# Performance work log

Measured on AMD Instinct MI355X. Metric: run time of the kernel, lower is better.

The kernel has to match this reference:

```python
import jax, jax.numpy as jnp
import numpy as np

L, H, P = 131072, 128, 128
STEP_RESCALE = 1.0
CONJ_SYM = True


def setup_inputs() -> dict:
    key = jax.random.key(0)
    ks = jax.random.split(key, 9)
    x = jax.random.normal(ks[0], (L, H), jnp.float32)
    # stable SSM: real parts of Lambda must be negative so |dA| < 1
    A_real_log = -(0.5 + jax.random.uniform(ks[1], (P,), jnp.float32))
    A_imag = 3.0 * jax.random.normal(ks[2], (P,), jnp.float32)
    B_re = jax.random.normal(ks[3], (P, H), jnp.float32) / np.sqrt(H)
    B_im = jax.random.normal(ks[4], (P, H), jnp.float32) / np.sqrt(H)
    C_re = jax.random.normal(ks[5], (H, P), jnp.float32) / np.sqrt(P)
    C_im = jax.random.normal(ks[6], (H, P), jnp.float32) / np.sqrt(P)
    D = jax.random.normal(ks[7], (H,), jnp.float32)
    # softplus(inv_dt) small -> small timestep dt
    inv_dt = jax.random.normal(ks[8], (P,), jnp.float32) - 4.0
    return {"x": x, "A_real_log": A_real_log, "A_imag": A_imag,
            "B_re": B_re, "B_im": B_im, "C_re": C_re, "C_im": C_im,
            "D": D, "inv_dt": inv_dt}


def reference(x, A_real_log, A_imag, B_re, B_im, C_re, C_im, D, inv_dt):
    # A = Lambda (diagonal complex state matrix), shape (P,)
    A = A_real_log + 1j * A_imag
    dt = STEP_RESCALE * jax.nn.softplus(inv_dt)            # (P,)
    # bilinear (Tustin) discretization
    BL = 1.0 / (1.0 - 0.5 * dt * A)                        # (P,)
    dA = BL * (1.0 + 0.5 * dt * A)                         # (P,)
    B = B_re + 1j * B_im                                   # (P,H)
    dB = (BL * dt)[:, None] * B                            # (P,H)
    # input projection into state space: (L,P) complex
    Bu = jnp.einsum('lh,ph->lp', x + 0j, dB)
    # linear recurrence h_k = dA * h_{k-1} + Bu_k via parallel associative scan
    A_elems = jnp.broadcast_to(dA[None, :], Bu.shape)
    def binop(q1, q2):
        a1, b1 = q1
        a2, b2 = q2
        return a1 * a2, a2 * b1 + b2
    _, hs = jax.lax.associative_scan(binop, (A_elems, Bu), axis=0)  # (L,P)
    C = C_re + 1j * C_im                                   # (H,P)
    y = jnp.einsum('lp,hp->lh', hs, C).real                # (L,H)
    if CONJ_SYM:
        y = 2.0 * y
    return y + x * D[None, :]
```

## Files before the change

kernel.cpp:

```cpp
#include <hip/hip_runtime.h>

#define L_LEN 131072
#define H_DIM 128
#define P_DIM 128
#define SEG 32
#define NSEG (L_LEN / SEG)
#define ROWS 64
#define NBLK (L_LEN / ROWS)

typedef unsigned int uint32;
typedef unsigned short u16;
typedef short bf16x8 __attribute__((ext_vector_type(8)));
typedef float f32x4 __attribute__((ext_vector_type(4)));

constexpr size_t OFF_DA  = 0;
constexpr size_t OFF_E   = OFF_DA + 256;
constexpr size_t OFF_HIN = OFF_E + (size_t)NSEG * 256;
constexpr size_t OFF_W1F = OFF_HIN + (size_t)NSEG * 256;
constexpr size_t OFF_W2F = OFF_W1F + 32768;

__device__ __forceinline__ u16 f2bf(float v) {
    uint32 u = __builtin_bit_cast(uint32, v);
    uint32 r = u + 0x7FFFu + ((u >> 16) & 1u);
    return (u16)(r >> 16);
}
__device__ __forceinline__ float bf2f(u16 h) {
    uint32 u = ((uint32)h) << 16;
    return __builtin_bit_cast(float, u);
}
__device__ __forceinline__ uint32 cvtpk(float lo, float hi) {
    uint32 r;
    asm("v_cvt_pk_bf16_f32 %0, %1, %2" : "=v"(r) : "v"(lo), "v"(hi));
    return r;
}
__device__ __forceinline__ float2 cfma(float2 a, float2 h, float2 c) {
    float2 r;
    r.x = fmaf(a.x, h.x, fmaf(-a.y, h.y, c.x));
    r.y = fmaf(a.x, h.y, fmaf(a.y, h.x, c.y));
    return r;
}
__device__ __forceinline__ float2 cmul(float2 a, float2 b) {
    return make_float2(fmaf(a.x, b.x, -a.y * b.y), fmaf(a.x, b.y, a.y * b.x));
}
__device__ __forceinline__ float2 unpk(uint32 w) {
    return make_float2(bf2f((u16)(w & 0xffffu)), bf2f((u16)(w >> 16)));
}

__global__ void k0(const float* __restrict__ Arl, const float* __restrict__ Ai,
                   const float* __restrict__ invdt,
                   const float* __restrict__ Bre, const float* __restrict__ Bim,
                   const float* __restrict__ Cre, const float* __restrict__ Cim,
                   float* __restrict__ dA,
                   u16* __restrict__ W1F, u16* __restrict__ W2F) {
    int tid = blockIdx.x * 256 + threadIdx.x;
    int lane = tid & 63;
    int fb = (tid >> 6) & 63;
    int ar = lane & 15, aq = lane >> 4;
    ushort4 hiA, hiB, loA, loB;
    u16* dst;
    if (tid < 4096) {
        int kt = fb >> 4, cf = fb & 15;
        int q = cf * 16 + ar;
        int p = q >> 1, c = q & 1;
        int h0 = kt * 32 + aq * 8;
        float idt = invdt[p];
        float dt = (idt > 20.f) ? idt : log1pf(expf(idt));
        float arl = Arl[p], aii = Ai[p];
        float zr = 0.5f * dt * arl, zi = 0.5f * dt * aii;
        float drr = 1.f - zr, dii = -zi;
        float inv = 1.f / (drr * drr + dii * dii);
        float blr = drr * inv, bli = -dii * inv;
        float2 s = make_float2(blr * dt, bli * dt);
        u16 hh[8], ll[8];
        #pragma unroll
        for (int j = 0; j < 8; ++j) {
            float br = Bre[p * H_DIM + h0 + j], bi = Bim[p * H_DIM + h0 + j];
            float re = fmaf(s.x, br, -s.y * bi);
            float im = fmaf(s.x, bi,  s.y * br);
            float v = c ? im : re;
            u16 h = f2bf(v); hh[j] = h; ll[j] = f2bf(v - bf2f(h));
        }
        hiA = make_ushort4(hh[0], hh[1], hh[2], hh[3]);
        hiB = make_ushort4(hh[4], hh[5], hh[6], hh[7]);
        loA = make_ushort4(ll[0], ll[1], ll[2], ll[3]);
        loB = make_ushort4(ll[4], ll[5], ll[6], ll[7]);
        dst = W1F + fb * 1024 + lane * 8;
    } else {
        int kk = fb >> 3, cf = fb & 7;
        int h = cf * 16 + ar;
        int q0 = kk * 32 + aq * 8;
        u16 hh[8], ll[8];
        #pragma unroll
        for (int j = 0; j < 8; ++j) {
            int q = q0 + j; int p = q >> 1;
            float v = (q & 1) ? (-2.f * Cim[h * P_DIM + p]) : (2.f * Cre[h * P_DIM + p]);
            u16 hv = f2bf(v); hh[j] = hv; ll[j] = f2bf(v - bf2f(hv));
        }
        hiA = make_ushort4(hh[0], hh[1], hh[2], hh[3]);
        hiB = make_ushort4(hh[4], hh[5], hh[6], hh[7]);
        loA = make_ushort4(ll[0], ll[1], ll[2], ll[3]);
        loB = make_ushort4(ll[4], ll[5], ll[6], ll[7]);
        dst = W2F + fb * 1024 + lane * 8;
    }
    *(ushort4*)(dst)       = hiA;
    *(ushort4*)(dst + 4)   = hiB;
    *(ushort4*)(dst + 512) = loA;
    *(ushort4*)(dst + 516) = loB;

    if (blockIdx.x == 0 && threadIdx.x < 128) {
        int p = threadIdx.x;
        float idt = invdt[p];
        float dt = (idt > 20.f) ? idt : log1pf(expf(idt));
        float arl = Arl[p], aii = Ai[p];
        float zr = 0.5f * dt * arl, zi = 0.5f * dt * aii;
        float drr = 1.f - zr, dii = -zi;
        float inv = 1.f / (drr * drr + dii * dii);
        float blr = drr * inv, bli = -dii * inv;
        float nr = 1.f + zr, ni = zi;
        dA[2 * p]     = fmaf(blr, nr, -bli * ni);
        dA[2 * p + 1] = fmaf(blr, ni,  bli * nr);
    }
}

__global__ __launch_bounds__(256) void k1(const float* __restrict__ x,
                                          const u16* __restrict__ W1F,
                                          const float* __restrict__ dA,
                                          float* __restrict__ E) {
    __shared__ __align__(16) char smem[32768];
    u16* As_hi = (u16*)smem;
    u16* SB    = (u16*)smem;
    int t = threadIdx.x, lane = t & 63, wid = t >> 6;
    size_t l0 = (size_t)blockIdx.x * ROWS;
    int ar = lane & 15, aq = lane >> 4, ak = aq * 8;

    bf16x8 bhp[4][4];
    #pragma unroll
    for (int kt = 0; kt < 4; ++kt)
        #pragma unroll
        for (int nf = 0; nf < 4; ++nf)
            bhp[kt][nf] = *(const bf16x8*)(W1F + (size_t)(kt * 16 + wid * 4 + nf) * 1024 + lane * 8);

    float4 xv[8];
    #pragma unroll
    for (int j = 0; j < 8; ++j) {
        int f = j * 256 + t; int row = f >> 5, c4 = f & 31;
        xv[j] = *(const float4*)(x + (l0 + row) * H_DIM + c4 * 4);
    }
    #pragma unroll
    for (int j = 0; j < 8; ++j) {
        int f = j * 256 + t; int row = f >> 5, c4 = f & 31;
        uint2 wv;
        wv.x = cvtpk(xv[j].x, xv[j].y);
        wv.y = cvtpk(xv[j].z, xv[j].w);
        *(uint2*)&As_hi[row * 136 + c4 * 4] = wv;
    }
    __syncthreads();

    f32x4 acc[4][4];
    #pragma unroll
    for (int a = 0; a < 4; ++a)
        #pragma unroll
        for (int b = 0; b < 4; ++b) acc[a][b] = (f32x4)0.f;
    #pragma unroll
    for (int kt = 0; kt < 4; ++kt) {
        bf16x8 ah[4];
        #pragma unroll
        for (int mf = 0; mf < 4; ++mf)
            ah[mf] = *(const bf16x8*)&As_hi[(mf * 16 + ar) * 136 + kt * 32 + ak];
        #pragma unroll
        for (int nf = 0; nf < 4; ++nf)
            #pragma unroll
            for (int mf = 0; mf < 4; ++mf)
                acc[mf][nf] = __builtin_amdgcn_mfma_f32_16x16x32_bf16(ah[mf], bhp[kt][nf], acc[mf][nf], 0, 0, 0);
    }
    __syncthreads();

    int sr = aq * 4;
    #pragma unroll
    for (int mf = 0; mf < 4; ++mf)
        #pragma unroll
        for (int nf = 0; nf < 4; ++nf) {
            int col = wid * 64 + nf * 16 + ar;
            uint32 w01 = cvtpk(acc[mf][nf][0], acc[mf][nf][1]);
            uint32 w23 = cvtpk(acc[mf][nf][2], acc[mf][nf][3]);
            int r0 = mf * 16 + sr;
            SB[(r0 + 0) * 256 + (((col >> 3) ^ ((r0 + 0) & 7)) << 3) + (col & 7)] = (u16)w01;
            SB[(r0 + 1) * 256 + (((col >> 3) ^ ((r0 + 1) & 7)) << 3) + (col & 7)] = (u16)(w01 >> 16);
            SB[(r0 + 2) * 256 + (((col >> 3) ^ ((r0 + 2) & 7)) << 3) + (col & 7)] = (u16)w23;
            SB[(r0 + 3) * 256 + (((col >> 3) ^ ((r0 + 3) & 7)) << 3) + (col & 7)] = (u16)(w23 >> 16);
        }
    __syncthreads();

    {
        int s = t >> 7, p = t & 127;
        float2 a = ((const float2*)dA)[p];
        uint32 buf[SEG];
        #pragma unroll
        for (int i = 0; i < SEG; ++i) {
            int row = s * 32 + i;
            buf[i] = *(const uint32*)&SB[row * 256 + (((p >> 2) ^ (row & 7)) << 3) + (p & 3) * 2];
        }
        float2 e = make_float2(0.f, 0.f);
        #pragma unroll
        for (int i = 0; i < SEG; ++i) e = cfma(a, e, unpk(buf[i]));
        ((float2*)E)[((size_t)blockIdx.x * 2 + s) * P_DIM + p] = e;
    }
}

__global__ __launch_bounds__(256) void k3(const float* __restrict__ E,
                                          const float* __restrict__ dA,
                                          float* __restrict__ Hin) {
    __shared__ float4 wagg[4];
    int m = blockIdx.x, t = threadIdx.x;
    int lane = t & 63, w = t >> 6;
    float2 aS = ((const float2*)dA)[m];
    #pragma unroll
    for (int i = 0; i < 5; ++i) aS = cmul(aS, aS);
    const float2* e = (const float2*)E;
    float2 ebuf[16];
    #pragma unroll
    for (int i = 0; i < 16; ++i) ebuf[i] = e[(size_t)(t * 16 + i) * P_DIM + m];
    float2 Bv = ebuf[0];
    #pragma unroll
    for (int i = 1; i < 16; ++i) Bv = cfma(aS, Bv, ebuf[i]);
    float2 Av = aS;
    #pragma unroll
    for (int i = 0; i < 4; ++i) Av = cmul(Av, Av);

    #pragma unroll
    for (int d = 1; d < 64; d <<= 1) {
        float uAx = __shfl_up(Av.x, (unsigned)d, 64);
        float uAy = __shfl_up(Av.y, (unsigned)d, 64);
        float uBx = __shfl_up(Bv.x, (unsigned)d, 64);
        float uBy = __shfl_up(Bv.y, (unsigned)d, 64);
        if (lane >= d) {
            float2 uA = make_float2(uAx, uAy), uB = make_float2(uBx, uBy);
            Bv = cfma(Av, uB, Bv);
            Av = cmul(uA, Av);
        }
    }
    if (lane == 63) wagg[w] = make_float4(Av.x, Av.y, Bv.x, Bv.y);
    __syncthreads();
    float2 Pb = make_float2(0.f, 0.f);
    for (int i = 0; i < w; ++i) {
        float4 u = wagg[i];
        float2 Wa = make_float2(u.x, u.y), Wb = make_float2(u.z, u.w);
        Pb = cfma(Wa, Pb, Wb);
    }
    float eAx = __shfl_up(Av.x, 1u, 64), eAy = __shfl_up(Av.y, 1u, 64);
    float eBx = __shfl_up(Bv.x, 1u, 64), eBy = __shfl_up(Bv.y, 1u, 64);
    float2 eA = make_float2(eAx, eAy), eB = make_float2(eBx, eBy);
    if (lane == 0) { eA = make_float2(1.f, 0.f); eB = make_float2(0.f, 0.f); }
    float2 pre = cfma(eA, Pb, eB);
    float2* hin = (float2*)Hin;
    #pragma unroll
    for (int i = 0; i < 16; ++i) {
        hin[(size_t)(t * 16 + i) * P_DIM + m] = pre;
        pre = cfma(aS, pre, ebuf[i]);
    }
}

__global__ __launch_bounds__(256) void k4(const float* __restrict__ x,
                                          const u16* __restrict__ W1F,
                                          const u16* __restrict__ W2F,
                                          const float* __restrict__ dA,
                                          const float* __restrict__ Hin,
                                          const float* __restrict__ Dv,
                                          float* __restrict__ y) {
    __shared__ __align__(16) char smem[33280];
    u16*   As_hi = (u16*)smem;
    u16*   SB    = (u16*)smem;
    float* SBF   = (float*)smem;
    int t = threadIdx.x, lane = t & 63, wid = t >> 6;
    size_t l0 = (size_t)blockIdx.x * ROWS;
    int ar = lane & 15, aq = lane >> 4, ak = aq * 8;

    bf16x8 bhp[4][4];
    #pragma unroll
    for (int kt = 0; kt < 4; ++kt)
        #pragma unroll
        for (int nf = 0; nf < 4; ++nf)
            bhp[kt][nf] = *(const bf16x8*)(W1F + (size_t)(kt * 16 + wid * 4 + nf) * 1024 + lane * 8);

    float4 xv[8];
    #pragma unroll
    for (int j = 0; j < 8; ++j) {
        int f = j * 256 + t; int row = f >> 5, c4 = f & 31;
        xv[j] = *(const float4*)(x + (l0 + row) * H_DIM + c4 * 4);
    }
    #pragma unroll
    for (int j = 0; j < 8; ++j) {
        int f = j * 256 + t; int row = f >> 5, c4 = f & 31;
        uint2 wv;
        wv.x = cvtpk(xv[j].x, xv[j].y);
        wv.y = cvtpk(xv[j].z, xv[j].w);
        *(uint2*)&As_hi[row * 136 + c4 * 4] = wv;
    }
    __syncthreads();

    {
        f32x4 acc[4][4];
        #pragma unroll
        for (int a = 0; a < 4; ++a)
            #pragma unroll
            for (int b = 0; b < 4; ++b) acc[a][b] = (f32x4)0.f;
        #pragma unroll
        for (int kt = 0; kt < 4; ++kt) {
            bf16x8 ah[4];
            #pragma unroll
            for (int mf = 0; mf < 4; ++mf)
                ah[mf] = *(const bf16x8*)&As_hi[(mf * 16 + ar) * 136 + kt * 32 + ak];
            #pragma unroll
            for (int nf = 0; nf < 4; ++nf)
                #pragma unroll
                for (int mf = 0; mf < 4; ++mf)
                    acc[mf][nf] = __builtin_amdgcn_mfma_f32_16x16x32_bf16(ah[mf], bhp[kt][nf], acc[mf][nf], 0, 0, 0);
        }
        __syncthreads();
        int sr = aq * 4;
        #pragma unroll
        for (int mf = 0; mf < 4; ++mf)
            #pragma unroll
            for (int nf = 0; nf < 4; ++nf) {
                int col = wid * 64 + nf * 16 + ar;
                uint32 w01 = cvtpk(acc[mf][nf][0], acc[mf][nf][1]);
                uint32 w23 = cvtpk(acc[mf][nf][2], acc[mf][nf][3]);
                int r0 = mf * 16 + sr;
                SB[(r0 + 0) * 256 + (((col >> 3) ^ ((r0 + 0) & 7)) << 3) + (col & 7)] = (u16)w01;
                SB[(r0 + 1) * 256 + (((col >> 3) ^ ((r0 + 1) & 7)) << 3) + (col & 7)] = (u16)(w01 >> 16);
                SB[(r0 + 2) * 256 + (((col >> 3) ^ ((r0 + 2) & 7)) << 3) + (col & 7)] = (u16)w23;
                SB[(r0 + 3) * 256 + (((col >> 3) ^ ((r0 + 3) & 7)) << 3) + (col & 7)] = (u16)(w23 >> 16);
            }
    }
    __syncthreads();

    bf16x8 bh2[8][2];
    #pragma unroll
    for (int kk = 0; kk < 8; ++kk)
        #pragma unroll
        for (int nf = 0; nf < 2; ++nf)
            bh2[kk][nf] = *(const bf16x8*)(W2F + (size_t)(kk * 8 + wid * 2 + nf) * 1024 + lane * 8);

    {
        int s = t >> 7, p = t & 127;
        float2 a = ((const float2*)dA)[p];
        float2 h = ((const float2*)Hin)[((size_t)blockIdx.x * 2 + s) * P_DIM + p];
        uint32 buf[SEG];
        #pragma unroll
        for (int i = 0; i < SEG; ++i) {
            int row = s * 32 + i;
            buf[i] = *(const uint32*)&SB[row * 256 + (((p >> 2) ^ (row & 7)) << 3) + (p & 3) * 2];
        }
        #pragma unroll
        for (int i = 0; i < SEG; ++i) {
            h = cfma(a, h, unpk(buf[i]));
            buf[i] = cvtpk(h.x, h.y);
        }
        #pragma unroll
        for (int i = 0; i < SEG; ++i) {
            int row = s * 32 + i;
            *(uint32*)&SB[row * 256 + (((p >> 2) ^ (row & 7)) << 3) + (p & 3) * 2] = buf[i];
        }
    }
    __syncthreads();

    f32x4 acc2[4][2];
    #pragma unroll
    for (int a = 0; a < 4; ++a)
        #pragma unroll
        for (int b = 0; b < 2; ++b) acc2[a][b] = (f32x4)0.f;
    #pragma unroll
    for (int kk = 0; kk < 8; ++kk) {
        bf16x8 af[4];
        #pragma unroll
        for (int mf = 0; mf < 4; ++mf) {
            int row = mf * 16 + ar;
            int blk = kk * 4 + aq;
            af[mf] = *(const bf16x8*)&SB[row * 256 + ((blk ^ (row & 7)) << 3)];
        }
        #pragma unroll
        for (int nf = 0; nf < 2; ++nf)
            #pragma unroll
            for (int mf = 0; mf < 4; ++mf)
                acc2[mf][nf] = __builtin_amdgcn_mfma_f32_16x16x32_bf16(af[mf], bh2[kk][nf], acc2[mf][nf], 0, 0, 0);
    }
    __syncthreads();

    int sr = aq * 4;
    #pragma unroll
    for (int mf = 0; mf < 4; ++mf)
        #pragma unroll
        for (int nf = 0; nf < 2; ++nf)
            #pragma unroll
            for (int r = 0; r < 4; ++r) {
                int row = mf * 16 + sr + r;
                int col = wid * 32 + nf * 16 + ar;
                SBF[row * 130 + col] = acc2[mf][nf][r];
            }
    __syncthreads();

    int c4 = t & 31;
    float4 dv = *(const float4*)(Dv + c4 * 4);
    #pragma unroll
    for (int j = 0; j < 8; ++j) {
        int row = j * 8 + (t >> 5);
        float4 sv = *(float4*)&SBF[row * 130 + c4 * 4];
        float4 out;
        out.x = fmaf(xv[j].x, dv.x, sv.x);
        out.y = fmaf(xv[j].y, dv.y, sv.y);
        out.z = fmaf(xv[j].z, dv.z, sv.z);
        out.w = fmaf(xv[j].w, dv.w, sv.w);
        *(float4*)(y + (l0 + row) * H_DIM + c4 * 4) = out;
    }
}

extern "C" void kernel_launch(void* const* d_in, const int* in_sizes, int n_in,
                              void* d_out, int out_size, void* d_ws, size_t ws_size,
                              hipStream_t stream) {
    const float* x     = (const float*)d_in[0];
    const float* Arl   = (const float*)d_in[1];
    const float* Ai    = (const float*)d_in[2];
    const float* Bre   = (const float*)d_in[3];
    const float* Bim   = (const float*)d_in[4];
    const float* Cre   = (const float*)d_in[5];
    const float* Cim   = (const float*)d_in[6];
    const float* Dv    = (const float*)d_in[7];
    const float* invdt = (const float*)d_in[8];
    float* y  = (float*)d_out;
    float* ws = (float*)d_ws;

    u16* w1f = (u16*)(ws + OFF_W1F);
    u16* w2f = (u16*)(ws + OFF_W2F);

    k0<<<32, 256, 0, stream>>>(Arl, Ai, invdt, Bre, Bim, Cre, Cim,
                               ws + OFF_DA, w1f, w2f);
    k1<<<NBLK, 256, 0, stream>>>(x, w1f, ws + OFF_DA, ws + OFF_E);
    k3<<<128, 256, 0, stream>>>(ws + OFF_E, ws + OFF_DA, ws + OFF_HIN);
    k4<<<NBLK, 256, 0, stream>>>(x, w1f, w2f, ws + OFF_DA,
                                 ws + OFF_HIN, Dv, y);
}
```

Before: 82.71 us.

## Compute segment end-states directly from MFMA registers via weighted power reduction

Replaces the LDS round-trip in k1, which wrote bf16 Bu tiles to shared memory and ran a 32-step sequential complex recurrence per state, with a closed-form weighted sum. Each MFMA accumulator element is multiplied by the matching power of dA for its row offset within the 32-row segment, then reduced with cross-lane shuffles. This removes two barriers, the LDS stores and loads, and the serial dependency chain. It also skips the bf16 rounding of Bu before the scan, which changes numerics slightly. Computing powers by repeated squaring may differ a little from the sequential recurrence in precision.

New measurement: 84.93 us. 2.7% more time.

```diff
diff --git a/kernel.cpp b/kernel.cpp
--- a/kernel.cpp
+++ b/kernel.cpp
@@ -126,9 +126,7 @@
                                           const u16* __restrict__ W1F,
                                           const float* __restrict__ dA,
                                           float* __restrict__ E) {
-    __shared__ __align__(16) char smem[32768];
-    u16* As_hi = (u16*)smem;
-    u16* SB    = (u16*)smem;
+    __shared__ __align__(16) u16 As_hi[64 * 136];
     int t = threadIdx.x, lane = t & 63, wid = t >> 6;
     size_t l0 = (size_t)blockIdx.x * ROWS;
     int ar = lane & 15, aq = lane >> 4, ak = aq * 8;
@@ -173,37 +171,38 @@
             for (int mf = 0; mf < 4; ++mf)
                 acc[mf][nf] = __builtin_amdgcn_mfma_f32_16x16x32_bf16(ah[mf], bhp[kt][nf], acc[mf][nf], 0, 0, 0);
     }
-    __syncthreads();
-
-    int sr = aq * 4;
-    #pragma unroll
-    for (int mf = 0; mf < 4; ++mf)
-        #pragma unroll
-        for (int nf = 0; nf < 4; ++nf) {
-            int col = wid * 64 + nf * 16 + ar;
-            uint32 w01 = cvtpk(acc[mf][nf][0], acc[mf][nf][1]);
-            uint32 w23 = cvtpk(acc[mf][nf][2], acc[mf][nf][3]);
-            int r0 = mf * 16 + sr;
-            SB[(r0 + 0) * 256 + (((col >> 3) ^ ((r0 + 0) & 7)) << 3) + (col & 7)] = (u16)w01;
-            SB[(r0 + 1) * 256 + (((col >> 3) ^ ((r0 + 1) & 7)) << 3) + (col & 7)] = (u16)(w01 >> 16);
-            SB[(r0 + 2) * 256 + (((col >> 3) ^ ((r0 + 2) & 7)) << 3) + (col & 7)] = (u16)w23;
-            SB[(r0 + 3) * 256 + (((col >> 3) ^ ((r0 + 3) & 7)) << 3) + (col & 7)] = (u16)(w23 >> 16);
-        }
-    __syncthreads();
-
-    {
-        int s = t >> 7, p = t & 127;
+
+    float sgn = (ar & 1) ? 1.f : -1.f;
+    #pragma unroll
+    for (int nf = 0; nf < 4; ++nf) {
+        int p = wid * 32 + nf * 8 + (ar >> 1);
         float2 a = ((const float2*)dA)[p];
-        uint32 buf[SEG];
-        #pragma unroll
-        for (int i = 0; i < SEG; ++i) {
-            int row = s * 32 + i;
-            buf[i] = *(const uint32*)&SB[row * 256 + (((p >> 2) ^ (row & 7)) << 3) + (p & 3) * 2];
-        }
-        float2 e = make_float2(0.f, 0.f);
-        #pragma unroll
-        for (int i = 0; i < SEG; ++i) e = cfma(a, e, unpk(buf[i]));
-        ((float2*)E)[((size_t)blockIdx.x * 2 + s) * P_DIM + p] = e;
+        float2 d2 = cmul(a, a), d3 = cmul(d2, a);
+        float2 D4 = cmul(d2, d2), D8 = cmul(D4, D4), P16 = cmul(D8, D8);
+        float2 D12 = cmul(D8, D4);
+        float2 Q = (aq == 0) ? D12 : (aq == 1) ? D8 : (aq == 2) ? D4 : make_float2(1.f, 0.f);
+        float2 QR[4];
+        QR[0] = cmul(Q, d3); QR[1] = cmul(Q, d2); QR[2] = cmul(Q, a); QR[3] = Q;
+        float2 WA[4];
+        #pragma unroll
+        for (int r = 0; r < 4; ++r) WA[r] = cmul(P16, QR[r]);
+        float e0 = 0.f, e1 = 0.f;
+        #pragma unroll
+        for (int mf = 0; mf < 4; ++mf)
+            #pragma unroll
+            for (int r = 0; r < 4; ++r) {
+                float own = acc[mf][nf][r];
+                float oth = __shfl_xor(own, 1, 64);
+                float2 w = (mf & 1) ? QR[r] : WA[r];
+                float tv = fmaf(w.x, own, sgn * w.y * oth);
+                if (mf < 2) e0 += tv; else e1 += tv;
+            }
+        e0 += __shfl_xor(e0, 16, 64); e0 += __shfl_xor(e0, 32, 64);
+        e1 += __shfl_xor(e1, 16, 64); e1 += __shfl_xor(e1, 32, 64);
+        if (aq == 0) {
+            E[(((size_t)blockIdx.x * 2 + 0) * P_DIM + p) * 2 + (ar & 1)] = e0;
+            E[(((size_t)blockIdx.x * 2 + 1) * P_DIM + p) * 2 + (ar & 1)] = e1;
+        }
     }
 }
 
```
